# Optimization experiments

Hardware: AMD Instinct MI355X
Metric: run time of the kernel (lower is better)

The kernel has to match this reference:

```python
import jax, jax.numpy as jnp
import numpy as np

IN_DIM, N_WIN, OUT_DIM = 128, 64, 128


def setup_inputs() -> dict:
    key = jax.random.key(0)
    kx, kw, kb = jax.random.split(key, 3)
    k = 1.0 / (IN_DIM * N_WIN)
    bound = float(np.sqrt(k))
    x = jax.random.normal(kx, (IN_DIM, 8192), dtype=jnp.float32)
    weight = jax.random.uniform(kw, (IN_DIM, N_WIN, OUT_DIM), dtype=jnp.float32,
                                minval=-bound, maxval=bound)
    bias = jax.random.uniform(kb, (OUT_DIM,), dtype=jnp.float32,
                              minval=-bound, maxval=bound)
    return {"x": x, "weight": weight, "bias": bias}


def reference(x, weight, bias):
    # x: (inDim, N); weight: (inDim, nWin, outDim); bias: (outDim,)
    # Original: TRFs[n,i,w,o] = x[n,i]*W[i,w,o] + bias[o], then sum over i.
    # Fused: out[n,w,o] = sum_i x[n,i]*W[i,w,o] + inDim*bias[o]
    in_dim = weight.shape[0]
    out = jnp.einsum('in,iwo->nwo', x, weight)
    out = out + in_dim * bias  # bias added before sum over inDim in original
    return out
```

## Files before the change

### kernel.cpp

```cpp
#include <hip/hip_runtime.h>
#include <hip/hip_bf16.h>
#include <stdint.h>

#define K_DIM 128
#define N_X   8192
#define N_WO  8192
#define OUT_TOTAL (8192UL * 64UL * 128UL)
#define CHUNKS_PER_PANEL 131072

typedef __attribute__((ext_vector_type(8))) short short8;
typedef __attribute__((ext_vector_type(4))) float f32x4;

__device__ inline unsigned short f2bf(float f) {
    union { float f; unsigned u; } v; v.f = f;
    unsigned u = v.u;
    u += 0x7fffu + ((u >> 16) & 1u);
    return (unsigned short)(u >> 16);
}

__global__ __launch_bounds__(256) void prep_frag2(const float* __restrict__ X,
                                                  const float* __restrict__ W,
                                                  uint4* __restrict__ Q) {
    int c  = blockIdx.x * 256 + threadIdx.x;
    int cc = c & (CHUNKS_PER_PANEL - 1);
    const float* P = (c >= CHUNKS_PER_PANEL) ? W : X;
    int l  = cc & 63;
    int ks = (cc >> 6) & 3;
    int t  = cc >> 8;
    int m  = t * 16 + (l & 15);
    int k0 = ks * 32 + ((l >> 4) << 3);
    const float* p = P + (size_t)k0 * N_X + m;
    unsigned short h[8];
#pragma unroll
    for (int j = 0; j < 8; ++j) h[j] = f2bf(p[(size_t)j * N_X]);
    uint4 q;
    q.x = (unsigned)h[0] | ((unsigned)h[1] << 16);
    q.y = (unsigned)h[2] | ((unsigned)h[3] << 16);
    q.z = (unsigned)h[4] | ((unsigned)h[5] << 16);
    q.w = (unsigned)h[6] | ((unsigned)h[7] << 16);
    Q[c] = q;
}

__global__ __launch_bounds__(256) void gemm_frag(const short8* __restrict__ A,
                                                 const short8* __restrict__ B,
                                                 const float* __restrict__ bias,
                                                 float* __restrict__ out) {
    int bid = blockIdx.x;
    int swz = (bid & 7) * 512 + (bid >> 3);
    int bm = swz >> 6, bn = swz & 63;

    int tid  = threadIdx.x;
    int lane = tid & 63;
    int w    = tid >> 6;
    int wr = w >> 1, wc = w & 1;
    int m0 = bm * 128 + wr * 64;
    int n0 = bn * 128 + wc * 64;
    int tm0 = m0 >> 4;
    int tn0 = n0 >> 4;

    f32x4 acc[4][4] = {};
#pragma unroll
    for (int ks = 0; ks < 4; ++ks) {
        short8 a[4], b[4];
#pragma unroll
        for (int i = 0; i < 4; ++i) {
            a[i] = A[((tm0 + i) * 4 + ks) * 64 + lane];
            b[i] = B[((tn0 + i) * 4 + ks) * 64 + lane];
        }
#pragma unroll
        for (int i = 0; i < 4; ++i)
#pragma unroll
            for (int j = 0; j < 4; ++j)
                acc[i][j] = __builtin_amdgcn_mfma_f32_16x16x32_bf16(
                    b[j], a[i], acc[i][j], 0, 0, 0);
    }

    int cl = lane & 15, rg = (lane >> 4) << 2;
#pragma unroll
    for (int i = 0; i < 4; ++i) {
        int nrow = m0 + i * 16 + cl;
        float* po_row = out + (size_t)nrow * N_WO;
#pragma unroll
        for (int j = 0; j < 4; ++j) {
            int wo = n0 + j * 16 + rg;
            const f32x4 bv = *(const f32x4*)(bias + (wo & 127));
            f32x4 v = acc[i][j];
            v.x = v.x + 128.0f * bv.x;
            v.y = v.y + 128.0f * bv.y;
            v.z = v.z + 128.0f * bv.z;
            v.w = v.w + 128.0f * bv.w;
            *(f32x4*)(po_row + wo) = v;
        }
    }
}

__global__ __launch_bounds__(256) void naive_kernel(const float* __restrict__ x,
                                                    const float* __restrict__ wgt,
                                                    const float* __restrict__ bias,
                                                    float* __restrict__ out) {
    size_t idx = (size_t)blockIdx.x * 256 + threadIdx.x;
    if (idx >= OUT_TOTAL) return;
    int n    = (int)(idx >> 13);
    int ncol = (int)(idx & 8191);
    float s = 0.f;
    for (int i = 0; i < K_DIM; ++i)
        s += x[(size_t)i * N_X + n] * wgt[(size_t)i * N_WO + ncol];
    out[idx] = s + 128.0f * bias[ncol & 127];
}

extern "C" void kernel_launch(void* const* d_in, const int* in_sizes, int n_in,
                              void* d_out, int out_size, void* d_ws, size_t ws_size,
                              hipStream_t stream) {
    const float* x    = (const float*)d_in[0];
    const float* wgt  = (const float*)d_in[1];
    const float* bias = (const float*)d_in[2];
    float* out = (float*)d_out;

    if (ws_size >= 4u * 1024u * 1024u) {
        uint4* wsA = (uint4*)d_ws;
        uint4* wsB = wsA + CHUNKS_PER_PANEL;
        prep_frag2<<<1024, 256, 0, stream>>>(x, wgt, wsA);
        gemm_frag<<<4096, 256, 0, stream>>>((const short8*)wsA, (const short8*)wsB,
                                            bias, out);
    } else {
        naive_kernel<<<(unsigned)((OUT_TOTAL + 255) / 256), 256, 0, stream>>>(
            x, wgt, bias, out);
    }
}
```

Before: 68.71 us.

## Stage 256x256 operand tiles in LDS via direct global-to-LDS loads

Replaces the register-only GEMM with 128x128 tiles by a 512-thread block computing 256x256 tiles. Full-K A and B panels are staged into 128KB of LDS with global_load_lds, and each wave then computes a 128x64 subtile from shared data. This is meant to cut redundant global and L2 operand traffic, since each fragment is now shared across more waves. The cost is 128KB of LDS per block, which limits occupancy to about one block per CU, plus a full barrier before any compute. The output write of 256MB still dominates, so the benefit may be small.

Result: faster. 67.19 us (-2.2%).

```diff
diff --git a/kernel.cpp b/kernel.cpp
--- a/kernel.cpp
+++ b/kernel.cpp
@@ -41,43 +41,63 @@
     Q[c] = q;
 }
 
-__global__ __launch_bounds__(256) void gemm_frag(const short8* __restrict__ A,
-                                                 const short8* __restrict__ B,
-                                                 const float* __restrict__ bias,
-                                                 float* __restrict__ out) {
+__global__ __launch_bounds__(512, 2) void gemm_lds(const uint4* __restrict__ A,
+                                                   const uint4* __restrict__ B,
+                                                   const float* __restrict__ bias,
+                                                   float* __restrict__ out) {
+    extern __shared__ uint4 lds[];
+    uint4* ldsA = lds;
+    uint4* ldsB = lds + 4096;
+
     int bid = blockIdx.x;
-    int swz = (bid & 7) * 512 + (bid >> 3);
-    int bm = swz >> 6, bn = swz & 63;
+    int swz = (bid & 7) * 128 + (bid >> 3);
+    int bm = swz >> 5, bn = swz & 31;
 
     int tid  = threadIdx.x;
     int lane = tid & 63;
     int w    = tid >> 6;
-    int wr = w >> 1, wc = w & 1;
-    int m0 = bm * 128 + wr * 64;
-    int n0 = bn * 128 + wc * 64;
-    int tm0 = m0 >> 4;
-    int tn0 = n0 >> 4;
+    int wr = w >> 2;
+    int wc = w & 3;
 
-    f32x4 acc[4][4] = {};
+    const uint4* gA = A + bm * 4096;
+    const uint4* gB = B + bn * 4096;
+#pragma unroll
+    for (int q = 0; q < 8; ++q) {
+        int c = (q * 8 + w) * 64;
+        __builtin_amdgcn_global_load_lds(
+            (const __attribute__((address_space(1))) void*)(gA + c + lane),
+            (__attribute__((address_space(3))) void*)(ldsA + c), 16, 0, 0);
+        __builtin_amdgcn_global_load_lds(
+            (const __attribute__((address_space(1))) void*)(gB + c + lane),
+            (__attribute__((address_space(3))) void*)(ldsB + c), 16, 0, 0);
+    }
+    __syncthreads();
+
+    const short8* fA = (const short8*)ldsA;
+    const short8* fB = (const short8*)ldsB;
+    f32x4 acc[8][4] = {};
 #pragma unroll
     for (int ks = 0; ks < 4; ++ks) {
-        short8 a[4], b[4];
+        short8 a[8], b[4];
 #pragma unroll
-        for (int i = 0; i < 4; ++i) {
-            a[i] = A[((tm0 + i) * 4 + ks) * 64 + lane];
-            b[i] = B[((tn0 + i) * 4 + ks) * 64 + lane];
-        }
+        for (int i = 0; i < 8; ++i)
+            a[i] = fA[((wr * 8 + i) * 4 + ks) * 64 + lane];
 #pragma unroll
-        for (int i = 0; i < 4; ++i)
+        for (int j = 0; j < 4; ++j)
+            b[j] = fB[((wc * 4 + j) * 4 + ks) * 64 + lane];
+#pragma unroll
+        for (int i = 0; i < 8; ++i)
 #pragma unroll
             for (int j = 0; j < 4; ++j)
                 acc[i][j] = __builtin_amdgcn_mfma_f32_16x16x32_bf16(
                     b[j], a[i], acc[i][j], 0, 0, 0);
     }
 
+    int m0 = bm * 256 + wr * 128;
+    int n0 = bn * 256 + wc * 64;
     int cl = lane & 15, rg = (lane >> 4) << 2;
 #pragma unroll
-    for (int i = 0; i < 4; ++i) {
+    for (int i = 0; i < 8; ++i) {
         int nrow = m0 + i * 16 + cl;
         float* po_row = out + (size_t)nrow * N_WO;
 #pragma unroll
@@ -120,8 +140,8 @@
         uint4* wsA = (uint4*)d_ws;
         uint4* wsB = wsA + CHUNKS_PER_PANEL;
         prep_frag2<<<1024, 256, 0, stream>>>(x, wgt, wsA);
-        gemm_frag<<<4096, 256, 0, stream>>>((const short8*)wsA, (const short8*)wsB,
-                                            bias, out);
+        gemm_lds<<<1024, 512, 131072, stream>>>((const uint4*)wsA, (const uint4*)wsB,
+                                                bias, out);
     } else {
         naive_kernel<<<(unsigned)((OUT_TOTAL + 255) / 256), 256, 0, stream>>>(
             x, wgt, bias, out);
```
